# Optimization experiments

Measured on AMD Instinct MI355X. Metric: run time of the kernel, lower is better.

## Reference

```python
import jax, jax.numpy as jnp
import numpy as np

NUM_HEADS = 12
DILATIONS = (1, 2, 4)
POOL_STRIDE = 2
LINFORMER_SEQ = 128


def setup_inputs() -> dict:
    key = jax.random.key(0)
    ks = jax.random.split(key, 8)
    B, N, C = 32, 1024, 768
    bank = 64
    return {
        "x": jax.random.normal(ks[0], (B, N, C), jnp.float32),
        "Wqkv": jax.random.normal(ks[1], (C, 3 * C), jnp.float32) * 0.02,
        "bqkv": jnp.zeros((3 * C,), jnp.float32),
        "E_k": jax.random.normal(ks[2], (LINFORMER_SEQ, 64), jnp.float32) * 0.02,
        "E_v": jax.random.normal(ks[3], (LINFORMER_SEQ, 64), jnp.float32) * 0.02,
        "Wproj": jax.random.normal(ks[4], (C, C), jnp.float32) * 0.02,
        "bproj": jnp.zeros((C,), jnp.float32),
        "k_bank": jax.random.normal(ks[5], (B, bank, C), jnp.float32),
        "v_bank": jax.random.normal(ks[6], (B, bank, C), jnp.float32),
    }


def reference(x, Wqkv, bqkv, E_k, E_v, Wproj, bproj, k_bank, v_bank):
    B, N, C = x.shape
    H = NUM_HEADS
    D = C // H
    S = int(np.sqrt(N))  # spatial side, N must be a perfect square

    # multi-scale dilated token gather
    xg = x.reshape(B, S, S, C)
    multi = [xg[:, ::d, ::d, :].reshape(B, -1, C) for d in DILATIONS]
    xm = jnp.concatenate(multi, axis=1)  # (B, NM, C)

    # landmark average pooling (kernel=stride=POOL_STRIDE, no padding)
    NM = xm.shape[1]
    NP = NM // POOL_STRIDE
    xp = xm[:, : NP * POOL_STRIDE].reshape(B, NP, POOL_STRIDE, C).mean(axis=2)

    # qkv on pooled landmarks, keep k and v heads
    qkv_p = (xp @ Wqkv + bqkv).reshape(B, NP, 3, H, D)
    k = qkv_p[:, :, 1].transpose(0, 2, 1, 3)  # (B,H,NP,D)
    v = qkv_p[:, :, 2].transpose(0, 2, 1, 3)

    # truncate/pad to Linformer seq_len (here NP=672 > 128 -> truncate)
    if k.shape[2] < LINFORMER_SEQ:
        pad = LINFORMER_SEQ - k.shape[2]
        k = jnp.pad(k, ((0, 0), (0, 0), (0, pad), (0, 0)))
        v = jnp.pad(v, ((0, 0), (0, 0), (0, pad), (0, 0)))
    else:
        k = k[:, :, :LINFORMER_SEQ]
        v = v[:, :, :LINFORMER_SEQ]

    # Linformer low-rank compression: E.T @ k
    kc = jnp.einsum('sc,bhsd->bhcd', E_k, k)  # (B,H,64,D)
    vc = jnp.einsum('sc,bhsd->bhcd', E_v, v)

    # memory bank heads
    kb = k_bank.reshape(B, -1, H, D).transpose(0, 2, 1, 3)
    vb = v_bank.reshape(B, -1, H, D).transpose(0, 2, 1, 3)
    k_full = jnp.concatenate([kc, kb], axis=2)  # (B,H,128,D)
    v_full = jnp.concatenate([vc, vb], axis=2)

    # queries from full-resolution tokens
    q = (x @ Wqkv + bqkv).reshape(B, N, 3, H, D)[:, :, 0].transpose(0, 2, 1, 3)

    # scaled dot-product attention (dropout p=0 in eval / reference)
    scale = 1.0 / jnp.sqrt(jnp.asarray(D, x.dtype))
    scores = jnp.einsum('bhqd,bhkd->bhqk', q, k_full) * scale
    attn = jax.nn.softmax(scores, axis=-1)
    out = jnp.einsum('bhqk,bhkd->bhqd', attn, v_full)

    out = out.transpose(0, 2, 1, 3).reshape(B, N, C)
    return out @ Wproj + bproj
```

## Files before the change

kernel.cpp:

```cpp
#include <hip/hip_runtime.h>

#define BB    32
#define NSEQ  1024
#define CDIM  768
#define NH    12
#define HD    64
#define LKEYS 128
#define NPOOL 128

typedef __bf16 bf16x8 __attribute__((ext_vector_type(8)));
typedef float  f32x4  __attribute__((ext_vector_type(4)));

__device__ __forceinline__ ushort f2bf(float f) {
    union { float f; uint u; } v; v.f = f;
    uint u = v.u;
    uint r = u + 0x7FFFu + ((u >> 16) & 1u);
    return (ushort)(r >> 16);
}
__device__ __forceinline__ uint pack2(float x, float y) {
    return (uint)f2bf(x) | ((uint)f2bf(y) << 16);
}

__global__ __launch_bounds__(256) void cvt_bf16_kernel(const float* __restrict__ src,
                                                       ushort* __restrict__ dst, int n8)
{
    int idx = blockIdx.x * 256 + threadIdx.x;
    if (idx >= n8) return;
    float4 a = ((const float4*)src)[idx * 2];
    float4 b = ((const float4*)src)[idx * 2 + 1];
    uint4 o;
    o.x = pack2(a.x, a.y); o.y = pack2(a.z, a.w);
    o.z = pack2(b.x, b.y); o.w = pack2(b.z, b.w);
    ((uint4*)dst)[idx] = o;
}

__global__ __launch_bounds__(256) void transpose_cvt_kernel(const float* __restrict__ src,
                                                            ushort* __restrict__ dst,
                                                            int R, int C)
{
    __shared__ ushort tile[32][33];
    int bc = blockIdx.x * 32, br = blockIdx.y * 32;
    int tx = threadIdx.x & 31, ty = threadIdx.x >> 5;
#pragma unroll
    for (int i = 0; i < 32; i += 8)
        tile[ty + i][tx] = f2bf(src[(size_t)(br + ty + i) * C + bc + tx]);
    __syncthreads();
#pragma unroll
    for (int i = 0; i < 32; i += 8)
        dst[(size_t)(bc + ty + i) * R + br + tx] = tile[tx][ty + i];
}

__global__ __launch_bounds__(256) void pool_kernel(const float* __restrict__ x,
                                                   ushort* __restrict__ xp)
{
    int idx = blockIdx.x * 256 + threadIdx.x;
    int c8 = idx % 96;
    int t  = idx / 96;
    int i  = t % NPOOL;
    int b  = t / NPOOL;
    if (b >= BB) return;
    const float4* x4 = (const float4*)x;
    size_t base0 = ((size_t)(b * NSEQ + 2 * i)) * 192 + c8 * 2;
    size_t base1 = base0 + 192;
    float4 a0 = x4[base0], a1 = x4[base0 + 1];
    float4 b0 = x4[base1], b1 = x4[base1 + 1];
    uint4 o;
    o.x = pack2(0.5f * (a0.x + b0.x), 0.5f * (a0.y + b0.y));
    o.y = pack2(0.5f * (a0.z + b0.z), 0.5f * (a0.w + b0.w));
    o.z = pack2(0.5f * (a1.x + b1.x), 0.5f * (a1.y + b1.y));
    o.w = pack2(0.5f * (a1.z + b1.z), 0.5f * (a1.w + b1.w));
    ((uint4*)xp)[idx] = o;
}

template <bool OBF16>
__global__ __launch_bounds__(256) void mfma_gemm_kernel(
    const ushort* __restrict__ A, const ushort* __restrict__ Bt,
    const float* __restrict__ bias, void* __restrict__ Cout,
    int M, int N, int K)
{
    __shared__ ushort As[128 * 32];
    __shared__ ushort Bs[128 * 32];

    int tid  = threadIdx.x;
    int wave = tid >> 6, lane = tid & 63;

    int nwg  = gridDim.x * gridDim.y;
    int bid  = blockIdx.y * gridDim.x + blockIdx.x;
    int q    = nwg >> 3, r = nwg & 7;
    int xcd  = bid & 7, j = bid >> 3;
    int flat = (xcd < r ? xcd * (q + 1) : r * (q + 1) + (xcd - r) * q) + j;
    int n0 = (flat % gridDim.x) * 128;
    int m0 = (flat / gridDim.x) * 128;

    int wm = wave >> 1, wn = wave & 1;
    int lm = lane & 15, lh = lane >> 4;

    f32x4 acc[4][4] = {};

    for (int k0 = 0; k0 < K; k0 += 32) {
        __syncthreads();
#pragma unroll
        for (int t = 0; t < 2; t++) {
            int fl = wave * 128 + t * 64 + lane;
            int row = fl >> 2, kc = (fl & 3) * 8;
            const ushort* gA = A  + (size_t)(m0 + row) * K + k0 + kc;
            const ushort* gB = Bt + (size_t)(n0 + row) * K + k0 + kc;
            __builtin_amdgcn_global_load_lds(
                (const __attribute__((address_space(1))) void*)gA,
                (__attribute__((address_space(3))) void*)(As + (size_t)(wave * 128 + t * 64) * 8),
                16, 0, 0);
            __builtin_amdgcn_global_load_lds(
                (const __attribute__((address_space(1))) void*)gB,
                (__attribute__((address_space(3))) void*)(Bs + (size_t)(wave * 128 + t * 64) * 8),
                16, 0, 0);
        }
        __syncthreads();

        bf16x8 af[4], bfr[4];
#pragma unroll
        for (int i = 0; i < 4; i++)
            af[i] = *(const bf16x8*)((const void*)&As[(wm * 64 + i * 16 + lm) * 32 + lh * 8]);
#pragma unroll
        for (int jj = 0; jj < 4; jj++)
            bfr[jj] = *(const bf16x8*)((const void*)&Bs[(wn * 64 + jj * 16 + lm) * 32 + lh * 8]);
#pragma unroll
        for (int i = 0; i < 4; i++)
#pragma unroll
            for (int jj = 0; jj < 4; jj++)
                acc[i][jj] = __builtin_amdgcn_mfma_f32_16x16x32_bf16(af[i], bfr[jj], acc[i][jj], 0, 0, 0);
    }

    int crow = m0 + wm * 64, ccol = n0 + wn * 64;
#pragma unroll
    for (int jj = 0; jj < 4; jj++) {
        int col = ccol + jj * 16 + lm;
        float bb = bias[col];
        if constexpr (OBF16) {
            ushort* C = (ushort*)Cout;
#pragma unroll
            for (int i = 0; i < 4; i++)
#pragma unroll
                for (int rr = 0; rr < 4; rr++)
                    C[(size_t)(crow + i * 16 + lh * 4 + rr) * N + col] = f2bf(acc[i][jj][rr] + bb);
        } else {
            float* C = (float*)Cout;
#pragma unroll
            for (int i = 0; i < 4; i++)
#pragma unroll
                for (int rr = 0; rr < 4; rr++)
                    C[(size_t)(crow + i * 16 + lh * 4 + rr) * N + col] = acc[i][jj][rr] + bb;
        }
    }
}

template <bool OBF16>
__global__ __launch_bounds__(512) void gemm256_kernel(
    const ushort* __restrict__ A, const ushort* __restrict__ Bt,
    const float* __restrict__ bias, void* __restrict__ Cout,
    int M, int N, int K)
{
    __shared__ ushort As[4][256 * 32];
    __shared__ ushort Bs[4][256 * 32];

    int tid  = threadIdx.x;
    int lane = tid & 63;
    int wave = tid >> 6;

    int nwg  = gridDim.x * gridDim.y;
    int bid  = blockIdx.y * gridDim.x + blockIdx.x;
    int q    = nwg >> 3, r = nwg & 7;
    int xcd  = bid & 7, j = bid >> 3;
    int flat = (xcd < r ? xcd * (q + 1) : r * (q + 1) + (xcd - r) * q) + j;
    int n0 = (flat % gridDim.x) * 256;
    int m0 = (flat / gridDim.x) * 256;

    int wm = wave >> 2, wn = wave & 3;
    int lm = lane & 15, lh = lane >> 4;

    int NT = K >> 5;

    auto stageA = [&](int tt) {
        int slot = tt & 3;
#pragma unroll
        for (int ld = 0; ld < 2; ld++) {
            int fl = ld * 512 + tid;
            int prow = fl >> 2, pch = fl & 3;
            int lch  = pch ^ ((prow >> 1) & 3);
            const ushort* g = A + (size_t)(m0 + prow) * K + tt * 32 + lch * 8;
            __builtin_amdgcn_global_load_lds(
                (const __attribute__((address_space(1))) void*)g,
                (__attribute__((address_space(3))) void*)(&As[slot][fl * 8]),
                16, 0, 0);
        }
    };
    auto stageB = [&](int tt) {
        int slot = tt & 3;
#pragma unroll
        for (int ld = 0; ld < 2; ld++) {
            int fl = ld * 512 + tid;
            int prow = fl >> 2, pch = fl & 3;
            int lch  = pch ^ ((prow >> 1) & 3);
            const ushort* g = Bt + (size_t)(n0 + prow) * K + tt * 32 + lch * 8;
            __builtin_amdgcn_global_load_lds(
                (const __attribute__((address_space(1))) void*)g,
                (__attribute__((address_space(3))) void*)(&Bs[slot][fl * 8]),
                16, 0, 0);
        }
    };

    f32x4 acc[8][4] = {};

    stageA(0); stageB(0);
    stageA(1); stageB(1);
    stageA(2); stageB(2);

    for (int t = 0; t < NT; t++) {
        int slot = t & 3;

        if (t + 3 < NT) stageA(t + 3);

        if (t + 3 < NT)       asm volatile("s_waitcnt vmcnt(10)" ::: "memory");
        else if (t + 3 == NT) asm volatile("s_waitcnt vmcnt(8)"  ::: "memory");
        else if (t + 2 == NT) asm volatile("s_waitcnt vmcnt(4)"  ::: "memory");
        else                  asm volatile("s_waitcnt vmcnt(0)"  ::: "memory");
        __builtin_amdgcn_s_barrier();
        asm volatile("" ::: "memory");

        bf16x8 bfrag[4], afrag[4];
#pragma unroll
        for (int jj = 0; jj < 4; jj++) {
            int rn = wn * 64 + jj * 16 + lm;
            int pch = lh ^ ((rn >> 1) & 3);
            bfrag[jj] = *(const bf16x8*)((const void*)&Bs[slot][rn * 32 + pch * 8]);
        }
#pragma unroll
        for (int i = 0; i < 4; i++) {
            int rm = wm * 128 + i * 16 + lm;
            int pch = lh ^ ((rm >> 1) & 3);
            afrag[i] = *(const bf16x8*)((const void*)&As[slot][rm * 32 + pch * 8]);
        }
        __builtin_amdgcn_s_setprio(1);
#pragma unroll
        for (int i = 0; i < 4; i++)
#pragma unroll
            for (int jj = 0; jj < 4; jj++)
                acc[i][jj] = __builtin_amdgcn_mfma_f32_16x16x32_bf16(afrag[i], bfrag[jj], acc[i][jj], 0, 0, 0);
        __builtin_amdgcn_s_setprio(0);
        __builtin_amdgcn_s_barrier();

        if (t + 3 < NT) stageB(t + 3);
#pragma unroll
        for (int i = 0; i < 4; i++) {
            int rm = wm * 128 + 64 + i * 16 + lm;
            int pch = lh ^ ((rm >> 1) & 3);
            afrag[i] = *(const bf16x8*)((const void*)&As[slot][rm * 32 + pch * 8]);
        }
        __builtin_amdgcn_s_setprio(1);
#pragma unroll
        for (int i = 0; i < 4; i++)
#pragma unroll
            for (int jj = 0; jj < 4; jj++)
                acc[4 + i][jj] = __builtin_amdgcn_mfma_f32_16x16x32_bf16(afrag[i], bfrag[jj], acc[4 + i][jj], 0, 0, 0);
        __builtin_amdgcn_s_setprio(0);
        __builtin_amdgcn_s_barrier();
    }

    int crow = m0 + wm * 128, ccol = n0 + wn * 64;
#pragma unroll
    for (int jj = 0; jj < 4; jj++) {
        int col = ccol + jj * 16 + lm;
        float bb = bias[col];
        if constexpr (OBF16) {
            ushort* C = (ushort*)Cout;
#pragma unroll
            for (int i = 0; i < 8; i++) {
                int rowb = crow + (i >> 2) * 64 + (i & 3) * 16 + lh * 4;
#pragma unroll
                for (int rr = 0; rr < 4; rr++)
                    C[(size_t)(rowb + rr) * N + col] = f2bf(acc[i][jj][rr] + bb);
            }
        } else {
            float* C = (float*)Cout;
#pragma unroll
            for (int i = 0; i < 8; i++) {
                int rowb = crow + (i >> 2) * 64 + (i & 3) * 16 + lh * 4;
#pragma unroll
                for (int rr = 0; rr < 4; rr++)
                    C[(size_t)(rowb + rr) * N + col] = acc[i][jj][rr] + bb;
            }
        }
    }
}

__global__ __launch_bounds__(256) void compress_kernel(
    const float* __restrict__ kvp,
    const float* __restrict__ Ek, const float* __restrict__ Ev,
    const float* __restrict__ kbank, const float* __restrict__ vbank,
    ushort* __restrict__ kfull, ushort* __restrict__ vfullT)
{
    __shared__ float Es[128 * 64];
    __shared__ float Sl[128 * 64];

    int tid = threadIdx.x;
    int h = blockIdx.x, b = blockIdx.y, which = blockIdx.z;
    const float* E    = which ? Ev : Ek;
    const float* bank = which ? vbank : kbank;

#pragma unroll
    for (int i = 0; i < 8; i++) {
        int flat = tid + i * 256;
        *(float4*)&Es[flat * 4] = *(const float4*)&E[flat * 4];
    }
    const float* src = kvp + (size_t)b * 128 * 1536 + which * 768 + h * HD;
#pragma unroll
    for (int i = 0; i < 8; i++) {
        int flat = tid + i * 256;
        int s = flat >> 4, d4 = flat & 15;
        *(float4*)&Sl[s * 64 + d4 * 4] = *(const float4*)&src[(size_t)s * 1536 + d4 * 4];
    }

    const float* bankbase = bank + (size_t)b * 64 * CDIM + h * HD;
    ushort* outK = kfull  + (size_t)(b * NH + h) * LKEYS * HD;
    ushort* outV = vfullT + (size_t)(b * NH + h) * HD * LKEYS;

#pragma unroll
    for (int i = 0; i < 4; i++) {
        int flat = tid + i * 256;
        int j = flat >> 4, d4 = flat & 15;
        float4 v = *(const float4*)&bankbase[(size_t)j * CDIM + d4 * 4];
        if (!which) {
            ushort4 o;
            o.x = f2bf(v.x); o.y = f2bf(v.y); o.z = f2bf(v.z); o.w = f2bf(v.w);
            *(ushort4*)&outK[(size_t)(64 + j) * HD + d4 * 4] = o;
        } else {
            outV[(size_t)(d4 * 4 + 0) * LKEYS + 64 + j] = f2bf(v.x);
            outV[(size_t)(d4 * 4 + 1) * LKEYS + 64 + j] = f2bf(v.y);
            outV[(size_t)(d4 * 4 + 2) * LKEYS + 64 + j] = f2bf(v.z);
            outV[(size_t)(d4 * 4 + 3) * LKEYS + 64 + j] = f2bf(v.w);
        }
    }
    __syncthreads();

    int tx = tid & 15, ty = tid >> 4;
    float acc[4][4];
#pragma unroll
    for (int i = 0; i < 4; i++)
#pragma unroll
        for (int j = 0; j < 4; j++) acc[i][j] = 0.f;

#pragma unroll 4
    for (int s = 0; s < 128; s++) {
        float4 av = *(const float4*)&Es[s * 64 + ty * 4];
        float4 bv = *(const float4*)&Sl[s * 64 + tx * 4];
        float a[4] = {av.x, av.y, av.z, av.w};
        float bb[4] = {bv.x, bv.y, bv.z, bv.w};
#pragma unroll
        for (int i = 0; i < 4; i++)
#pragma unroll
            for (int j = 0; j < 4; j++)
                acc[i][j] += a[i] * bb[j];
    }
    if (!which) {
#pragma unroll
        for (int i = 0; i < 4; i++) {
            ushort4 o;
            o.x = f2bf(acc[i][0]); o.y = f2bf(acc[i][1]);
            o.z = f2bf(acc[i][2]); o.w = f2bf(acc[i][3]);
            *(ushort4*)&outK[(size_t)(ty * 4 + i) * HD + tx * 4] = o;
        }
    } else {
#pragma unroll
        for (int i = 0; i < 4; i++)
#pragma unroll
            for (int j = 0; j < 4; j++)
                outV[(size_t)(tx * 4 + j) * LKEYS + ty * 4 + i] = f2bf(acc[i][j]);
    }
}

__global__ __launch_bounds__(256) void attn_mfma_kernel(
    const ushort* __restrict__ qb, const ushort* __restrict__ kf,
    const ushort* __restrict__ vt, ushort* __restrict__ ob)
{
    __shared__ __align__(16) ushort lds[64 * 72 + 128 * 72 + 64 * 136];
    ushort* Qs = lds;
    ushort* Ks = lds + 64 * 72;
    ushort* Vs = lds + 64 * 72 + 128 * 72;
    ushort* Ps = lds;

    int tid  = threadIdx.x;
    int wave = tid >> 6, lane = tid & 63;
    int lm = lane & 15, lh = lane >> 4;
    int qt = blockIdx.x, h = blockIdx.y, b = blockIdx.z;

    const ushort* qbase = qb + ((size_t)(b * NSEQ + qt * 64)) * CDIM + h * HD;
    const ushort* kbase = kf + (size_t)(b * NH + h) * LKEYS * HD;
    const ushort* vbase = vt + (size_t)(b * NH + h) * HD * LKEYS;

#pragma unroll
    for (int it = 0; it < 2; it++) {
        int flat = tid + it * 256;
        int row = flat >> 3, seg = flat & 7;
        *(uint4*)&Qs[row * 72 + seg * 8] = *(const uint4*)&qbase[(size_t)row * CDIM + seg * 8];
    }
#pragma unroll
    for (int it = 0; it < 4; it++) {
        int flat = tid + it * 256;
        int row = flat >> 3, seg = flat & 7;
        *(uint4*)&Ks[row * 72 + seg * 8] = *(const uint4*)&kbase[(size_t)row * HD + seg * 8];
    }
#pragma unroll
    for (int it = 0; it < 4; it++) {
        int flat = tid + it * 256;
        int row = flat >> 4, seg = flat & 15;
        *(uint4*)&Vs[row * 136 + seg * 8] = *(const uint4*)&vbase[(size_t)row * LKEYS + seg * 8];
    }
    __syncthreads();

    f32x4 sacc[8] = {};
    bf16x8 aq[2];
#pragma unroll
    for (int ks = 0; ks < 2; ks++)
        aq[ks] = *(const bf16x8*)((const void*)&Qs[(wave * 16 + lm) * 72 + ks * 32 + lh * 8]);
#pragma unroll
    for (int j = 0; j < 8; j++)
#pragma unroll
        for (int ks = 0; ks < 2; ks++) {
            bf16x8 bk = *(const bf16x8*)((const void*)&Ks[(j * 16 + lm) * 72 + ks * 32 + lh * 8]);
            sacc[j] = __builtin_amdgcn_mfma_f32_16x16x32_bf16(aq[ks], bk, sacc[j], 0, 0, 0);
        }

    float rinv[4];
#pragma unroll
    for (int r = 0; r < 4; r++) {
        float m = sacc[0][r];
#pragma unroll
        for (int j = 1; j < 8; j++) m = fmaxf(m, sacc[j][r]);
#pragma unroll
        for (int off = 1; off < 16; off <<= 1) m = fmaxf(m, __shfl_xor(m, off, 64));
        float s = 0.f;
#pragma unroll
        for (int j = 0; j < 8; j++) {
            float e = __expf((sacc[j][r] - m) * 0.125f);
            sacc[j][r] = e;
            s += e;
        }
#pragma unroll
        for (int off = 1; off < 16; off <<= 1) s += __shfl_xor(s, off, 64);
        rinv[r] = 1.f / s;
    }

    __syncthreads();
#pragma unroll
    for (int j = 0; j < 8; j++)
#pragma unroll
        for (int r = 0; r < 4; r++)
            Ps[(size_t)(wave * 16 + lh * 4 + r) * 136 + j * 16 + lm] = f2bf(sacc[j][r] * rinv[r]);
    __syncthreads();

    f32x4 oacc[4] = {};
#pragma unroll
    for (int ks = 0; ks < 4; ks++) {
        bf16x8 ap = *(const bf16x8*)((const void*)&Ps[(wave * 16 + lm) * 136 + ks * 32 + lh * 8]);
#pragma unroll
        for (int j = 0; j < 4; j++) {
            bf16x8 bv = *(const bf16x8*)((const void*)&Vs[(j * 16 + lm) * 136 + ks * 32 + lh * 8]);
            oacc[j] = __builtin_amdgcn_mfma_f32_16x16x32_bf16(ap, bv, oacc[j], 0, 0, 0);
        }
    }

    ushort* obase = ob + ((size_t)(b * NSEQ + qt * 64)) * CDIM + h * HD;
#pragma unroll
    for (int j = 0; j < 4; j++)
#pragma unroll
        for (int r = 0; r < 4; r++)
            obase[(size_t)(wave * 16 + lh * 4 + r) * CDIM + j * 16 + lm] = f2bf(oacc[j][r]);
}

extern "C" void kernel_launch(void* const* d_in, const int* in_sizes, int n_in,
                              void* d_out, int out_size, void* d_ws, size_t ws_size,
                              hipStream_t stream)
{
    const float* x     = (const float*)d_in[0];
    const float* Wqkv  = (const float*)d_in[1];
    const float* bqkv  = (const float*)d_in[2];
    const float* Ek    = (const float*)d_in[3];
    const float* Ev    = (const float*)d_in[4];
    const float* Wproj = (const float*)d_in[5];
    const float* bproj = (const float*)d_in[6];
    const float* kbank = (const float*)d_in[7];
    const float* vbank = (const float*)d_in[8];
    float* out = (float*)d_out;
    float* ws  = (float*)d_ws;

    float*  kvp    = ws;
    ushort* qb_bf  = (ushort*)ws;
    ushort* x_bf   = (ushort*)(ws + 12582912);
    ushort* aob    = x_bf;
    ushort* xp_bf  = (ushort*)(ws + 25165824);
    ushort* Wq_t   = (ushort*)(ws + 26738688);
    ushort* Wp_t   = (ushort*)(ws + 27623424);
    ushort* k_full = (ushort*)(ws + 27918336);
    ushort* v_fullT= (ushort*)(ws + 29491200);

    cvt_bf16_kernel<<<12288, 256, 0, stream>>>(x, x_bf, 3145728);
    transpose_cvt_kernel<<<dim3(72, 24), 256, 0, stream>>>(Wqkv, Wq_t, CDIM, 3 * CDIM);
    transpose_cvt_kernel<<<dim3(24, 24), 256, 0, stream>>>(Wproj, Wp_t, CDIM, CDIM);
    pool_kernel<<<1536, 256, 0, stream>>>(x, xp_bf);

    mfma_gemm_kernel<false><<<dim3(12, 32), 256, 0, stream>>>(
        xp_bf, Wq_t + (size_t)CDIM * CDIM, bqkv + CDIM, kvp, 4096, 2 * CDIM, CDIM);
    compress_kernel<<<dim3(NH, BB, 2), 256, 0, stream>>>(
        kvp, Ek, Ev, kbank, vbank, k_full, v_fullT);

    gemm256_kernel<true><<<dim3(3, 128), 512, 0, stream>>>(
        x_bf, Wq_t, bqkv, qb_bf, BB * NSEQ, CDIM, CDIM);

    attn_mfma_kernel<<<dim3(16, NH, BB), 256, 0, stream>>>(qb_bf, k_full, v_fullT, aob);

    gemm256_kernel<false><<<dim3(3, 128), 512, 0, stream>>>(
        aob, Wp_t, bproj, out, BB * NSEQ, CDIM, CDIM);
}
```

Baseline: 443.9 us.

## Switch big GEMMs to 256x128 tiles with BK=64 triple-buffered pipeline

Replaces the 256x256, BK=32, four-stage GEMM used for the Q projection and the output projection with a 256x128 tile, BK=64, three-stage kernel. The LDS swizzle changes to an 8-chunk XOR pattern, each wave computes a 64x64 sub-tile, and the grid doubles to 768 workgroups. The aim is fewer barriers per K step and better CU occupancy and load balance across the 256 CUs. In exchange, each workgroup reuses less data and each wave does less MFMA work per fragment load.

After: 405.4 us. -8.7%, faster.

```diff
diff --git a/kernel.cpp b/kernel.cpp
--- a/kernel.cpp
+++ b/kernel.cpp
@@ -154,13 +154,13 @@
 }
 
 template <bool OBF16>
-__global__ __launch_bounds__(512) void gemm256_kernel(
+__global__ __launch_bounds__(512) void gemm_bk64_kernel(
     const ushort* __restrict__ A, const ushort* __restrict__ Bt,
     const float* __restrict__ bias, void* __restrict__ Cout,
     int M, int N, int K)
 {
-    __shared__ ushort As[4][256 * 32];
-    __shared__ ushort Bs[4][256 * 32];
+    __shared__ ushort As[3][256 * 64];
+    __shared__ ushort Bs[3][128 * 64];
 
     int tid  = threadIdx.x;
     int lane = tid & 63;
@@ -169,38 +169,35 @@
     int nwg  = gridDim.x * gridDim.y;
     int bid  = blockIdx.y * gridDim.x + blockIdx.x;
     int q    = nwg >> 3, r = nwg & 7;
-    int xcd  = bid & 7, j = bid >> 3;
-    int flat = (xcd < r ? xcd * (q + 1) : r * (q + 1) + (xcd - r) * q) + j;
-    int n0 = (flat % gridDim.x) * 256;
+    int xcd  = bid & 7, jj0 = bid >> 3;
+    int flat = (xcd < r ? xcd * (q + 1) : r * (q + 1) + (xcd - r) * q) + jj0;
+    int n0 = (flat % gridDim.x) * 128;
     int m0 = (flat / gridDim.x) * 256;
 
-    int wm = wave >> 2, wn = wave & 3;
+    int wm = wave >> 1, wn = wave & 1;
     int lm = lane & 15, lh = lane >> 4;
 
-    int NT = K >> 5;
-
-    auto stageA = [&](int tt) {
-        int slot = tt & 3;
-#pragma unroll
-        for (int ld = 0; ld < 2; ld++) {
+    int NT = K >> 6;
+
+    auto stage = [&](int tt) {
+        int slot = tt - (tt / 3) * 3;
+#pragma unroll
+        for (int ld = 0; ld < 4; ld++) {
             int fl = ld * 512 + tid;
-            int prow = fl >> 2, pch = fl & 3;
-            int lch  = pch ^ ((prow >> 1) & 3);
-            const ushort* g = A + (size_t)(m0 + prow) * K + tt * 32 + lch * 8;
+            int prow = fl >> 3, pch = fl & 7;
+            int lch  = pch ^ (prow & 7);
+            const ushort* g = A + (size_t)(m0 + prow) * K + tt * 64 + lch * 8;
             __builtin_amdgcn_global_load_lds(
                 (const __attribute__((address_space(1))) void*)g,
                 (__attribute__((address_space(3))) void*)(&As[slot][fl * 8]),
                 16, 0, 0);
         }
-    };
-    auto stageB = [&](int tt) {
-        int slot = tt & 3;
 #pragma unroll
         for (int ld = 0; ld < 2; ld++) {
             int fl = ld * 512 + tid;
-            int prow = fl >> 2, pch = fl & 3;
-            int lch  = pch ^ ((prow >> 1) & 3);
-            const ushort* g = Bt + (size_t)(n0 + prow) * K + tt * 32 + lch * 8;
+            int prow = fl >> 3, pch = fl & 7;
+            int lch  = pch ^ (prow & 7);
+            const ushort* g = Bt + (size_t)(n0 + prow) * K + tt * 64 + lch * 8;
             __builtin_amdgcn_global_load_lds(
                 (const __attribute__((address_space(1))) void*)g,
                 (__attribute__((address_space(3))) void*)(&Bs[slot][fl * 8]),
@@ -208,64 +205,52 @@
         }
     };
 
-    f32x4 acc[8][4] = {};
-
-    stageA(0); stageB(0);
-    stageA(1); stageB(1);
-    stageA(2); stageB(2);
+    f32x4 acc[4][4] = {};
+
+    stage(0);
+    stage(1);
 
     for (int t = 0; t < NT; t++) {
-        int slot = t & 3;
-
-        if (t + 3 < NT) stageA(t + 3);
-
-        if (t + 3 < NT)       asm volatile("s_waitcnt vmcnt(10)" ::: "memory");
-        else if (t + 3 == NT) asm volatile("s_waitcnt vmcnt(8)"  ::: "memory");
-        else if (t + 2 == NT) asm volatile("s_waitcnt vmcnt(4)"  ::: "memory");
+        int slot = t - (t / 3) * 3;
+
+        if (t + 2 < NT) stage(t + 2);
+
+        if (t + 2 < NT)       asm volatile("s_waitcnt vmcnt(12)" ::: "memory");
+        else if (t + 2 == NT) asm volatile("s_waitcnt vmcnt(6)"  ::: "memory");
         else                  asm volatile("s_waitcnt vmcnt(0)"  ::: "memory");
         __builtin_amdgcn_s_barrier();
         asm volatile("" ::: "memory");
 
-        bf16x8 bfrag[4], afrag[4];
-#pragma unroll
-        for (int jj = 0; jj < 4; jj++) {
-            int rn = wn * 64 + jj * 16 + lm;
-            int pch = lh ^ ((rn >> 1) & 3);
-            bfrag[jj] = *(const bf16x8*)((const void*)&Bs[slot][rn * 32 + pch * 8]);
-        }
-#pragma unroll
-        for (int i = 0; i < 4; i++) {
-            int rm = wm * 128 + i * 16 + lm;
-            int pch = lh ^ ((rm >> 1) & 3);
-            afrag[i] = *(const bf16x8*)((const void*)&As[slot][rm * 32 + pch * 8]);
-        }
-        __builtin_amdgcn_s_setprio(1);
-#pragma unroll
-        for (int i = 0; i < 4; i++)
-#pragma unroll
-            for (int jj = 0; jj < 4; jj++)
-                acc[i][jj] = __builtin_amdgcn_mfma_f32_16x16x32_bf16(afrag[i], bfrag[jj], acc[i][jj], 0, 0, 0);
-        __builtin_amdgcn_s_setprio(0);
+        bf16x8 bfr[2][4];
+#pragma unroll
+        for (int ks = 0; ks < 2; ks++)
+#pragma unroll
+            for (int jj = 0; jj < 4; jj++) {
+                int rn = wn * 64 + jj * 16 + lm;
+                int ch = (ks * 4 + lh) ^ (rn & 7);
+                bfr[ks][jj] = *(const bf16x8*)((const void*)&Bs[slot][rn * 64 + ch * 8]);
+            }
+#pragma unroll
+        for (int ks = 0; ks < 2; ks++) {
+            bf16x8 af[4];
+#pragma unroll
+            for (int i = 0; i < 4; i++) {
+                int rm = wm * 64 + i * 16 + lm;
+                int ch = (ks * 4 + lh) ^ (rm & 7);
+                af[i] = *(const bf16x8*)((const void*)&As[slot][rm * 64 + ch * 8]);
+            }
+            __builtin_amdgcn_s_setprio(1);
+#pragma unroll
+            for (int i = 0; i < 4; i++)
+#pragma unroll
+                for (int jj = 0; jj < 4; jj++)
+                    acc[i][jj] = __builtin_amdgcn_mfma_f32_16x16x32_bf16(af[i], bfr[ks][jj], acc[i][jj], 0, 0, 0);
+            __builtin_amdgcn_s_setprio(0);
+        }
         __builtin_amdgcn_s_barrier();
-
-        if (t + 3 < NT) stageB(t + 3);
-#pragma unroll
-        for (int i = 0; i < 4; i++) {
-            int rm = wm * 128 + 64 + i * 16 + lm;
-            int pch = lh ^ ((rm >> 1) & 3);
-            afrag[i] = *(const bf16x8*)((const void*)&As[slot][rm * 32 + pch * 8]);
-        }
-        __builtin_amdgcn_s_setprio(1);
-#pragma unroll
-        for (int i = 0; i < 4; i++)
-#pragma unroll
-            for (int jj = 0; jj < 4; jj++)
-                acc[4 + i][jj] = __builtin_amdgcn_mfma_f32_16x16x32_bf16(afrag[i], bfrag[jj], acc[4 + i][jj], 0, 0, 0);
-        __builtin_amdgcn_s_setprio(0);
-        __builtin_amdgcn_s_barrier();
-    }
-
-    int crow = m0 + wm * 128, ccol = n0 + wn * 64;
+    }
+
+    int crow = m0 + wm * 64, ccol = n0 + wn * 64;
 #pragma unroll
     for (int jj = 0; jj < 4; jj++) {
         int col = ccol + jj * 16 + lm;
@@ -273,21 +258,17 @@
         if constexpr (OBF16) {
             ushort* C = (ushort*)Cout;
 #pragma unroll
-            for (int i = 0; i < 8; i++) {
-                int rowb = crow + (i >> 2) * 64 + (i & 3) * 16 + lh * 4;
+            for (int i = 0; i < 4; i++)
 #pragma unroll
                 for (int rr = 0; rr < 4; rr++)
-                    C[(size_t)(rowb + rr) * N + col] = f2bf(acc[i][jj][rr] + bb);
-            }
+                    C[(size_t)(crow + i * 16 + lh * 4 + rr) * N + col] = f2bf(acc[i][jj][rr] + bb);
         } else {
             float* C = (float*)Cout;
 #pragma unroll
-            for (int i = 0; i < 8; i++) {
-                int rowb = crow + (i >> 2) * 64 + (i & 3) * 16 + lh * 4;
+            for (int i = 0; i < 4; i++)
 #pragma unroll
                 for (int rr = 0; rr < 4; rr++)
-                    C[(size_t)(rowb + rr) * N + col] = acc[i][jj][rr] + bb;
-            }
+                    C[(size_t)(crow + i * 16 + lh * 4 + rr) * N + col] = acc[i][jj][rr] + bb;
         }
     }
 }
@@ -512,11 +493,11 @@
     compress_kernel<<<dim3(NH, BB, 2), 256, 0, stream>>>(
         kvp, Ek, Ev, kbank, vbank, k_full, v_fullT);
 
-    gemm256_kernel<true><<<dim3(3, 128), 512, 0, stream>>>(
+    gemm_bk64_kernel<true><<<dim3(6, 128), 512, 0, stream>>>(
         x_bf, Wq_t, bqkv, qb_bf, BB * NSEQ, CDIM, CDIM);
 
     attn_mfma_kernel<<<dim3(16, NH, BB), 256, 0, stream>>>(qb_bf, k_full, v_fullT, aob);
 
-    gemm256_kernel<false><<<dim3(3, 128), 512, 0, stream>>>(
+    gemm_bk64_kernel<false><<<dim3(6, 128), 512, 0, stream>>>(
         aob, Wp_t, bproj, out, BB * NSEQ, CDIM, CDIM);
 }
```
